# Optimization experiments

Hardware: AMD Instinct MI355X
Metric: run time of the kernel (lower is better)

## Reference

```python
import jax, jax.numpy as jnp
import numpy as np

B, IMG, TXT, DIM, H, D = 1, 1024, 256, 1536, 24, 64
SCALE = 1.0  # control cross-attn scale


def _lin(x, w, b):
    return x @ w + b


def _heads(x):  # [B,S,DIM] -> [B,H,S,D]
    return jnp.swapaxes(x.reshape(x.shape[0], x.shape[1], H, D), 1, 2)


def _merge(x):  # [B,H,S,D] -> [B,S,DIM]
    return jnp.swapaxes(x, 1, 2).reshape(x.shape[0], x.shape[2], H * D)


def _sdpa(q, k, v):
    s = jnp.einsum('bhqd,bhkd->bhqk', q, k) * (1.0 / np.sqrt(D))
    return jnp.einsum('bhqk,bhkd->bhqd', jax.nn.softmax(s, axis=-1), v)


def _rope(x, pe):  # x: [B,H,S,D], pe: [1,1,S,D//2,2,2]
    xr = x.reshape(*x.shape[:-1], -1, 1, 2)  # [B,H,S,D/2,1,2]
    out = pe[..., 0] * xr[..., 0] + pe[..., 1] * xr[..., 1]  # [B,H,S,D/2,2]
    return out.reshape(x.shape)


def _forward(hidden_states, encoder_hidden_states, hidden_states_control,
             encoder_hidden_states_control, img_to_q_control, pe,
             a_q_w, a_q_b, a_k_w, a_k_b, a_v_w, a_v_b,
             a_addq_w, a_addq_b, a_addk_w, a_addk_b, a_addv_w, a_addv_b,
             a_out_w, a_out_b, a_addout_w, a_addout_b,
             c_q_w, c_q_b, c_k_w, c_k_b, c_v_w, c_v_b,
             c_addq_w, c_addq_b, c_addk_w, c_addk_b, c_addv_w, c_addv_b,
             c_out_w, c_out_b, c_addout_w, c_addout_b):
    img_len = hidden_states.shape[1]
    # ---- main joint attention stream (no RoPE, per original) ----
    q = jnp.concatenate([_heads(_lin(hidden_states, a_q_w, a_q_b)),
                         _heads(_lin(encoder_hidden_states, a_addq_w, a_addq_b))], axis=2)
    k = jnp.concatenate([_heads(_lin(hidden_states, a_k_w, a_k_b)),
                         _heads(_lin(encoder_hidden_states, a_addk_w, a_addk_b))], axis=2)
    v = jnp.concatenate([_heads(_lin(hidden_states, a_v_w, a_v_b)),
                         _heads(_lin(encoder_hidden_states, a_addv_w, a_addv_b))], axis=2)
    hs = _merge(_sdpa(q, k, v))
    hs, ehs = hs[:, :img_len], hs[:, img_len:]
    # ---- control joint attention stream (with RoPE) ----
    qc = jnp.concatenate([_heads(_lin(hidden_states_control, c_q_w, c_q_b)),
                          _heads(_lin(encoder_hidden_states_control, c_addq_w, c_addq_b))], axis=2)
    kc = jnp.concatenate([_heads(_lin(hidden_states_control, c_k_w, c_k_b)),
                          _heads(_lin(encoder_hidden_states_control, c_addk_w, c_addk_b))], axis=2)
    vc = jnp.concatenate([_heads(_lin(hidden_states_control, c_v_w, c_v_b)),
                          _heads(_lin(encoder_hidden_states_control, c_addv_w, c_addv_b))], axis=2)
    key_cross, value_cross = kc, vc  # saved BEFORE RoPE, per original
    hsc = _merge(_sdpa(_rope(qc, pe), _rope(kc, pe), vc))
    hsc, ehsc = hsc[:, :img_len], hsc[:, img_len:]
    # ---- cross attention: img query attends to control K/V ----
    q_cross = _rope(_heads(img_to_q_control), pe[:, :, :img_len])
    k_cross = _rope(key_cross, pe[:, :, :key_cross.shape[2]])
    cross = _merge(_sdpa(q_cross, k_cross, value_cross))
    hs = hs + SCALE * cross
    # ---- output projections (to_out[1] is dropout p=0 -> identity) ----
    hs = _lin(hs, a_out_w, a_out_b)
    ehs = _lin(ehs, a_addout_w, a_addout_b)
    hsc = _lin(hsc, c_out_w, c_out_b)
    ehsc = _lin(ehsc, c_addout_w, c_addout_b)
    return hs, ehs, hsc, ehsc


def setup_inputs() -> dict:
    key = jax.random.key(0)
    ki = iter(jax.random.split(key, 80))
    d = {}
    d['hidden_states'] = jax.random.normal(next(ki), (B, IMG, DIM), jnp.float32)
    d['encoder_hidden_states'] = jax.random.normal(next(ki), (B, TXT, DIM), jnp.float32)
    d['hidden_states_control'] = jax.random.normal(next(ki), (B, IMG, DIM), jnp.float32)
    d['encoder_hidden_states_control'] = jax.random.normal(next(ki), (B, TXT, DIM), jnp.float32)
    d['img_to_q_control'] = jax.random.normal(next(ki), (B, IMG, DIM), jnp.float32)
    # realistic rotary pe: [1,1,S,D/2,2,2] rotation matrices
    S = IMG + TXT
    pos = np.arange(S, dtype=np.float32)
    freqs = 1.0 / (10000.0 ** (np.arange(0, D, 2, dtype=np.float32) / D))  # [D/2]
    ang = pos[:, None] * freqs[None, :]  # [S, D/2]
    cos, sin = np.cos(ang), np.sin(ang)
    pe = np.stack([np.stack([cos, -sin], -1), np.stack([sin, cos], -1)], -2)  # [S,D/2,2,2]
    d['pe'] = jnp.asarray(pe)[None, None]
    for p in ('a', 'c'):
        for name in ('q', 'k', 'v', 'addq', 'addk', 'addv', 'out', 'addout'):
            d[f'{p}_{name}_w'] = jax.random.normal(next(ki), (DIM, DIM), jnp.float32) * 0.02
            d[f'{p}_{name}_b'] = jax.random.normal(next(ki), (DIM,), jnp.float32) * 0.01
    return d


def reference(hidden_states, encoder_hidden_states, hidden_states_control,
              encoder_hidden_states_control, img_to_q_control, pe,
              a_q_w, a_q_b, a_k_w, a_k_b, a_v_w, a_v_b,
              a_addq_w, a_addq_b, a_addk_w, a_addk_b, a_addv_w, a_addv_b,
              a_out_w, a_out_b, a_addout_w, a_addout_b,
              c_q_w, c_q_b, c_k_w, c_k_b, c_v_w, c_v_b,
              c_addq_w, c_addq_b, c_addk_w, c_addk_b, c_addv_w, c_addv_b,
              c_out_w, c_out_b, c_addout_w, c_addout_b):
    return _forward(hidden_states, encoder_hidden_states, hidden_states_control,
                    encoder_hidden_states_control, img_to_q_control, pe,
                    a_q_w, a_q_b, a_k_w, a_k_b, a_v_w, a_v_b,
                    a_addq_w, a_addq_b, a_addk_w, a_addk_b, a_addv_w, a_addv_b,
                    a_out_w, a_out_b, a_addout_w, a_addout_b,
                    c_q_w, c_q_b, c_k_w, c_k_b, c_v_w, c_v_b,
                    c_addq_w, c_addq_b, c_addk_w, c_addk_b, c_addv_w, c_addv_b,
                    c_out_w, c_out_b, c_addout_w, c_addout_b)
```

## Files before the change

kernel.cpp:

```cpp
#include <hip/hip_runtime.h>

#define DIM 1536
#define IMG 1024
#define TXT 256
#define SEQ 1280
#define NH 24
#define HD 64
#define SD ((size_t)SEQ * DIM)
#define IDSZ ((size_t)IMG * DIM)
#define WSZ ((size_t)DIM * DIM)

typedef __attribute__((ext_vector_type(8))) short short8;
typedef __attribute__((ext_vector_type(4))) float f32x4;

__device__ __forceinline__ float bf2f(ushort u) {
    union { unsigned int i; float f; } v; v.i = ((unsigned int)u) << 16; return v.f;
}
__device__ __forceinline__ ushort f2bf(float f) {
    union { unsigned int i; float f; } v; v.f = f;
    unsigned int u = v.i;
    u += 0x7fffu + ((u >> 16) & 1u);
    return (ushort)(u >> 16);
}

__global__ __launch_bounds__(256) void detect_dtype(const void* __restrict__ p,
                                                    int* __restrict__ flag)
{
    __shared__ int cnt;
    if (threadIdx.x == 0) cnt = 0;
    __syncthreads();
    const ushort* u = (const ushort*)p;
    int local = 0;
    for (int i = threadIdx.x; i < 2048; i += 256) {
        ushort v = u[2 * i];
        int e = (v >> 7) & 0xFF;
        if (e >= 0xC0) local++;
    }
    atomicAdd(&cnt, local);
    __syncthreads();
    if (threadIdx.x == 0) flag[0] = (cnt > 16) ? 1 : 0;
}

struct CvtP {
    const void* src[20];
    ushort* dst[20];
    int n8[20];
};

__global__ __launch_bounds__(256) void convert_bf16(CvtP p, const int* __restrict__ dflag)
{
    const int a = blockIdx.y;
    const int i = blockIdx.x * 256 + threadIdx.x;
    if (i >= p.n8[a]) return;
    const size_t off = (size_t)i * 8;
    uint4 o;
    if (dflag[0]) {
        const float* s = (const float*)p.src[a] + off;
        const float4 f0 = *(const float4*)s;
        const float4 f1 = *(const float4*)(s + 4);
        ushort t[8];
        t[0] = f2bf(f0.x); t[1] = f2bf(f0.y); t[2] = f2bf(f0.z); t[3] = f2bf(f0.w);
        t[4] = f2bf(f1.x); t[5] = f2bf(f1.y); t[6] = f2bf(f1.z); t[7] = f2bf(f1.w);
        o = *(uint4*)t;
    } else {
        o = *(const uint4*)((const ushort*)p.src[a] + off);
    }
    *(uint4*)(p.dst[a] + off) = o;
}

#define LSTR 40

struct QKV3P {
    const ushort* Xb;
    const ushort* Wb;
    const void* B[12];
    float* Y[6];
    ushort* Yh[6];
    ushort* Yl[6];
};

__global__ __launch_bounds__(256) void gemm_qkv_v4(QKV3P p, const int* __restrict__ dflag)
{
    __shared__ __align__(16) ushort As[2][128 * LSTR];
    __shared__ __align__(16) ushort Bs[2][64 * 64];
    const int dt = dflag[0];
    const int bx = blockIdx.x;
    const int wsel = bx / 12;
    const int n0 = (bx - wsel * 12) * 128;
    const int ys = blockIdx.y;
    const int str = (ys >= 10) ? 1 : 0;
    const int m0g = (ys - str * 10) * 128;
    const bool istxt = (m0g >= IMG);
    const int widx = str * 6 + wsel + (istxt ? 3 : 0);
    const ushort* X  = p.Xb + (size_t)str * SD;
    const ushort* Wp = p.Wb + (size_t)widx * WSZ;
    const void* Bp = p.B[widx];
    const int yidx = str * 3 + wsel;
    float*  Y  = p.Y[yidx];
    ushort* yh = p.Yh[yidx];
    ushort* yl = p.Yl[yidx];

    const int t = threadIdx.x;
    const int wave = t >> 6, lane = t & 63;
    const int quad = lane >> 4, l16 = lane & 15;
    const int wm = (wave >> 1) * 64, wn = (wave & 1) * 64;

    const int arow = t >> 1, apair = t & 1;
    const int bn8 = (t & 15) << 3, bkk = (t >> 4) << 1;
    const int aps = apair ^ ((arow >> 3) & 1);
    const int adst = arow * LSTR + aps * 16;
    const int bkg = bkk >> 3, bo = bkk & 7;

    f32x4 acc[4][4];
#pragma unroll
    for (int i = 0; i < 4; ++i)
#pragma unroll
        for (int j = 0; j < 4; ++j) acc[i][j] = (f32x4)(0.0f);

    uint4 rau[2];
    uint4 rbu[2];

    auto loadA = [&](int k0) {
        const ushort* xp = X + (size_t)(m0g + arow) * DIM + k0 + apair * 16;
        rau[0] = *(const uint4*)xp;
        rau[1] = *(const uint4*)(xp + 8);
    };
    auto loadB = [&](int k0) {
        const ushort* wp0 = Wp + (size_t)(k0 + bkk) * DIM + n0 + bn8;
        rbu[0] = *(const uint4*)wp0;
        rbu[1] = *(const uint4*)(wp0 + DIM);
    };
    auto storeA = [&](int buf) {
        *(uint4*)&As[buf][adst]     = rau[0];
        *(uint4*)&As[buf][adst + 8] = rau[1];
    };
    auto storeB = [&](int buf) {
        ushort t0[8], t1[8];
        *(uint4*)t0 = rbu[0];
        *(uint4*)t1 = rbu[1];
#pragma unroll
        for (int j = 0; j < 8; ++j) {
            const int rr = bn8 + j;
            const int R = rr & 63, half = rr >> 6;
            const int gx = (((half << 2) + bkg) ^ (R & 7) ^ (R >> 3)) & 7;
            *(unsigned int*)&Bs[buf][R * 64 + gx * 8 + bo] =
                (unsigned int)t0[j] | ((unsigned int)t1[j] << 16);
        }
    };

    loadA(0); loadB(0);
    storeA(0); storeB(0);
    __syncthreads();

    for (int k = 0; k < DIM / 32; ++k) {
        const int cur = k & 1;
        const bool hn = (k + 1) < DIM / 32;
        if (hn) { loadA((k + 1) * 32); loadB((k + 1) * 32); }

        short8 b[4];
#pragma unroll
        for (int j = 0; j < 4; ++j) {
            const int rrn = wn + j * 16 + l16;
            const int R = rrn & 63, half = rrn >> 6;
            const int gx = (((half << 2) + quad) ^ (R & 7) ^ (R >> 3)) & 7;
            b[j] = *(const short8*)&Bs[cur][R * 64 + gx * 8];
        }
#pragma unroll
        for (int i = 0; i < 4; ++i) {
            const int rr = wm + i * 16 + l16;
            const int ps = (quad >> 1) ^ ((rr >> 3) & 1);
            const int col = ps * 16 + (quad & 1) * 8;
            short8 a = *(const short8*)&As[cur][rr * LSTR + col];
#pragma unroll
            for (int j = 0; j < 4; ++j)
                acc[i][j] = __builtin_amdgcn_mfma_f32_16x16x32_bf16(a, b[j], acc[i][j], 0, 0, 0);
        }
        if (hn) { storeA(cur ^ 1); storeB(cur ^ 1); }
        __syncthreads();
    }

#pragma unroll
    for (int j = 0; j < 4; ++j) {
        const int col = n0 + wn + j * 16 + l16;
        const float bv = dt ? ((const float*)Bp)[col] : bf2f(((const ushort*)Bp)[col]);
#pragma unroll
        for (int i = 0; i < 4; ++i)
#pragma unroll
            for (int r = 0; r < 4; ++r) {
                const int row = m0g + wm + i * 16 + quad * 4 + r;
                const size_t o = (size_t)row * DIM + col;
                const float val = acc[i][j][r] + bv;
                if (Y) Y[o] = val;
                if (yh) {
                    const ushort hv = f2bf(val);
                    yh[o] = hv;
                    yl[o] = f2bf(val - bf2f(hv));
                }
            }
    }
}

struct OutP {
    const ushort* Xh; const ushort* Xl;
    const ushort* Wb;
    const void* B[4];
    void* out;
};

__global__ __launch_bounds__(256) void gemm_out_v4(OutP p, const int* __restrict__ dflag)
{
    __shared__ __align__(16) ushort Ah[2][64 * LSTR];
    __shared__ __align__(16) ushort Al[2][64 * LSTR];
    __shared__ __align__(16) ushort Bs[2][64 * 64];
    const int dt = dflag[0];
    const int n0 = blockIdx.x * 128;
    const int mt = blockIdx.y;
    const int seg = (mt < 16) ? 0 : (mt < 20) ? 1 : (mt < 36) ? 2 : 3;
    const ushort* Wp = p.Wb + (size_t)seg * WSZ;
    const void* Bp = p.B[seg];
    const int m0 = mt * 64;

    const int t = threadIdx.x;
    const int wave = t >> 6, lane = t & 63;
    const int quad = lane >> 4, l16 = lane & 15;
    const int wm = (wave >> 1) * 32, wn = (wave & 1) * 64;

    const int arow = t >> 2, ag = t & 3;
    const int apg = ag >> 1, asub = ag & 1;
    const int aps = apg ^ ((arow >> 3) & 1);
    const int adst = arow * LSTR + aps * 16 + asub * 8;
    const int bn8 = (t & 15) << 3, bkk = (t >> 4) << 1;
    const int bkg = bkk >> 3, bo = bkk & 7;

    f32x4 acc[2][4];
#pragma unroll
    for (int i = 0; i < 2; ++i)
#pragma unroll
        for (int j = 0; j < 4; ++j) acc[i][j] = (f32x4)(0.0f);

    uint4 rah, ral;
    uint4 rbu[2];

    auto loadA = [&](int k0) {
        const size_t off = (size_t)(m0 + arow) * DIM + k0 + ag * 8;
        rah = *(const uint4*)(p.Xh + off);
        ral = *(const uint4*)(p.Xl + off);
    };
    auto loadB = [&](int k0) {
        const ushort* wp0 = Wp + (size_t)(k0 + bkk) * DIM + n0 + bn8;
        rbu[0] = *(const uint4*)wp0;
        rbu[1] = *(const uint4*)(wp0 + DIM);
    };
    auto storeA = [&](int buf) {
        *(uint4*)&Ah[buf][adst] = rah;
        *(uint4*)&Al[buf][adst] = ral;
    };
    auto storeB = [&](int buf) {
        ushort t0[8], t1[8];
        *(uint4*)t0 = rbu[0];
        *(uint4*)t1 = rbu[1];
#pragma unroll
        for (int j = 0; j < 8; ++j) {
            const int rr = bn8 + j;
            const int R = rr & 63, half = rr >> 6;
            const int gx = (((half << 2) + bkg) ^ (R & 7) ^ (R >> 3)) & 7;
            *(unsigned int*)&Bs[buf][R * 64 + gx * 8 + bo] =
                (unsigned int)t0[j] | ((unsigned int)t1[j] << 16);
        }
    };

    loadA(0); loadB(0);
    storeA(0); storeB(0);
    __syncthreads();

    for (int k = 0; k < DIM / 32; ++k) {
        const int cur = k & 1;
        const bool hn = (k + 1) < DIM / 32;
        if (hn) { loadA((k + 1) * 32); loadB((k + 1) * 32); }

        short8 b[4];
#pragma unroll
        for (int j = 0; j < 4; ++j) {
            const int rrn = wn + j * 16 + l16;
            const int R = rrn & 63, half = rrn >> 6;
            const int gx = (((half << 2) + quad) ^ (R & 7) ^ (R >> 3)) & 7;
            b[j] = *(const short8*)&Bs[cur][R * 64 + gx * 8];
        }
#pragma unroll
        for (int i = 0; i < 2; ++i) {
            const int rr = wm + i * 16 + l16;
            const int ps = (quad >> 1) ^ ((rr >> 3) & 1);
            const int col = ps * 16 + (quad & 1) * 8;
            short8 ah = *(const short8*)&Ah[cur][rr * LSTR + col];
            short8 al = *(const short8*)&Al[cur][rr * LSTR + col];
#pragma unroll
            for (int j = 0; j < 4; ++j) {
                acc[i][j] = __builtin_amdgcn_mfma_f32_16x16x32_bf16(ah, b[j], acc[i][j], 0, 0, 0);
                acc[i][j] = __builtin_amdgcn_mfma_f32_16x16x32_bf16(al, b[j], acc[i][j], 0, 0, 0);
            }
        }
        if (hn) { storeA(cur ^ 1); storeB(cur ^ 1); }
        __syncthreads();
    }

#pragma unroll
    for (int j = 0; j < 4; ++j) {
        const int col = n0 + wn + j * 16 + l16;
        const float bv = dt ? ((const float*)Bp)[col] : bf2f(((const ushort*)Bp)[col]);
#pragma unroll
        for (int i = 0; i < 2; ++i)
#pragma unroll
            for (int r = 0; r < 4; ++r) {
                const int grow = m0 + wm + i * 16 + quad * 4 + r;
                const size_t o = (size_t)grow * DIM + col;
                const float val = acc[i][j][r] + bv;
                if (dt) ((float*)p.out)[o] = val;
                else    ((ushort*)p.out)[o] = f2bf(val);
            }
    }
}

__device__ __forceinline__ void pe_load(const void* pe, int dt, size_t off,
                                        float& c00, float& c01, float& c10, float& c11)
{
    if (dt) {
        float4 pv = *(const float4*)((const float*)pe + off);
        c00 = pv.x; c01 = pv.y; c10 = pv.z; c11 = pv.w;
    } else {
        const ushort* pp = (const ushort*)pe + off;
        c00 = bf2f(pp[0]); c01 = bf2f(pp[1]); c10 = bf2f(pp[2]); c11 = bf2f(pp[3]);
    }
}

struct PrepP {
    const float* v1; const float* vC;
    ushort *vthA, *vtlA, *vthC, *vtlC;
    float* q1;
    const float* k1; ushort *khC, *kloC;
    const void* i2q; float* qx;
    const void* pe;
};

#define VT_BLKS 960
#define RN0 (SEQ * 768)
#define RN1 (SEQ * 768)
#define RN2 (IMG * 768)

__global__ __launch_bounds__(256) void prep_fused(PrepP p, const int* __restrict__ dflag)
{
    __shared__ unsigned int tile[64 * 65];
    const int dt = dflag[0];
    const int bx = blockIdx.x;
    const int t = threadIdx.x;

    if (bx < VT_BLKS) {
        const int z = bx / 480, rem = bx - z * 480;
        const int s0 = (rem % 20) * 64, h = rem / 20;
        const float* V = z ? p.vC : p.v1;
        ushort* Vth = z ? p.vthC : p.vthA;
        ushort* Vtl = z ? p.vtlC : p.vtlA;
#pragma unroll
        for (int it = 0; it < 16; ++it) {
            const int sl = (t >> 6) + (it << 2);
            const int d = t & 63;
            const float v = V[(size_t)(s0 + sl) * DIM + h * HD + d];
            const ushort hv = f2bf(v);
            const ushort lv = f2bf(v - bf2f(hv));
            tile[d * 65 + sl] = (unsigned int)hv | ((unsigned int)lv << 16);
        }
        __syncthreads();
        const int d = t >> 2, cc = (t & 3) << 4;
        ushort th[16], tl[16];
#pragma unroll
        for (int j = 0; j < 16; ++j) {
            const unsigned int w = tile[d * 65 + cc + j];
            th[j] = (ushort)w;
            tl[j] = (ushort)(w >> 16);
        }
        const size_t off = (size_t)(h * HD + d) * SEQ + s0 + cc;
        *(uint4*)(Vth + off)     = *(uint4*)&th[0];
        *(uint4*)(Vth + off + 8) = *(uint4*)&th[8];
        *(uint4*)(Vtl + off)     = *(uint4*)&tl[0];
        *(uint4*)(Vtl + off + 8) = *(uint4*)&tl[8];
        return;
    }

    int idx = (bx - VT_BLKS) * 256 + t;
    if (idx < RN0) {
        int s = idx / 768, pp = idx - s * 768;
        int col = pp << 1, i = pp & 31;
        float* bp = p.q1 + (size_t)s * DIM + col;
        float x0 = bp[0], x1 = bp[1];
        float c00, c01, c10, c11;
        pe_load(p.pe, dt, (size_t)s * 128 + i * 4, c00, c01, c10, c11);
        bp[0] = c00 * x0 + c01 * x1;
        bp[1] = c10 * x0 + c11 * x1;
        return;
    }
    idx -= RN0;
    if (idx < RN1) {
        int s = idx / 768, pp = idx - s * 768;
        int col = pp << 1, i = pp & 31;
        float2 xv = *(const float2*)(p.k1 + (size_t)s * DIM + col);
        float c00, c01, c10, c11;
        pe_load(p.pe, dt, (size_t)s * 128 + i * 4, c00, c01, c10, c11);
        float y0 = c00 * xv.x + c01 * xv.y;
        float y1 = c10 * xv.x + c11 * xv.y;
        ushort h0 = f2bf(y0), h1 = f2bf(y1);
        ushort l0 = f2bf(y0 - bf2f(h0)), l1 = f2bf(y1 - bf2f(h1));
        *(unsigned int*)(p.khC  + (size_t)s * DIM + col) = (unsigned int)h0 | ((unsigned int)h1 << 16);
        *(unsigned int*)(p.kloC + (size_t)s * DIM + col) = (unsigned int)l0 | ((unsigned int)l1 << 16);
        return;
    }
    idx -= RN1;
    if (idx < RN2) {
        int s = idx / 768, pp = idx - s * 768;
        int col = pp << 1, i = pp & 31;
        float x0, x1;
        if (dt) {
            float2 xv = *(const float2*)((const float*)p.i2q + (size_t)s * DIM + col);
            x0 = xv.x; x1 = xv.y;
        } else {
            const ushort* sp = (const ushort*)p.i2q + (size_t)s * DIM + col;
            x0 = bf2f(sp[0]); x1 = bf2f(sp[1]);
        }
        float c00, c01, c10, c11;
        pe_load(p.pe, dt, (size_t)s * 128 + i * 4, c00, c01, c10, c11);
        float* dp = p.qx + (size_t)s * DIM + col;
        dp[0] = c00 * x0 + c01 * x1;
        dp[1] = c10 * x0 + c11 * x1;
    }
}

__device__ __forceinline__ int swz(int row, int col) {
    return row * 64 + ((((col >> 3) ^ row) & 7) << 3) + (col & 7);
}
__device__ __forceinline__ short8 ldfrag(const ushort* plane, int row, int col) {
    return *(const short8*)&plane[swz(row, col)];
}

struct AttnAllP {
    const float* Qf[3];
    const ushort* Kh[3]; const ushort* Kl[3];
    const ushort* Vth[3]; const ushort* Vtl[3];
    float* Op0[3]; float* Op1[3];
    float2* Ml[3];
    int mlq[3];
};

__global__ __launch_bounds__(256) void attn_all(AttnAllP p)
{
    __shared__ ushort Qh_[4096], Ql_[4096];
    __shared__ ushort Kh_[4096], Kl_[4096];
    __shared__ ushort Vh_[4096], Vl_[4096];

    const int bx = blockIdx.x;
    const int seg = (bx < 20) ? 0 : (bx < 40) ? 1 : 2;
    const int q0 = (bx - ((seg == 0) ? 0 : (seg == 1) ? 20 : 40)) * 64;
    const int h = blockIdx.y;
    const int z = blockIdx.z;
    const int t = threadIdx.x;
    const int wave = t >> 6, lane = t & 63;
    const int quad = lane >> 4, l16 = lane & 15;
    const int wq0 = wave * 16;

    const float* Qf = p.Qf[seg];
    const ushort* Kh = p.Kh[seg]; const ushort* Kl = p.Kl[seg];
    const ushort* Vth = p.Vth[seg]; const ushort* Vtl = p.Vtl[seg];

    const int srow = t >> 2, c0 = (t & 3) << 4;
    const int g0 = c0 >> 3;
    const int p0 = ((g0 ^ (srow & 7)) & 7) << 3;
    const int p1 = (((g0 + 1) ^ (srow & 7)) & 7) << 3;

    {
        const float* src = Qf + (size_t)(q0 + srow) * DIM + h * HD + c0;
        float x[16];
        *(float4*)&x[0]  = *(const float4*)(src);
        *(float4*)&x[4]  = *(const float4*)(src + 4);
        *(float4*)&x[8]  = *(const float4*)(src + 8);
        *(float4*)&x[12] = *(const float4*)(src + 12);
        ushort hi[16], lo[16];
#pragma unroll
        for (int i = 0; i < 16; ++i) {
            hi[i] = f2bf(x[i]);
            lo[i] = f2bf(x[i] - bf2f(hi[i]));
        }
        *(uint4*)&Qh_[srow * 64 + p0] = *(uint4*)&hi[0];
        *(uint4*)&Qh_[srow * 64 + p1] = *(uint4*)&hi[8];
        *(uint4*)&Ql_[srow * 64 + p0] = *(uint4*)&lo[0];
        *(uint4*)&Ql_[srow * 64 + p1] = *(uint4*)&lo[8];
    }
    short8 qfh[2], qfl[2];
#pragma unroll
    for (int c = 0; c < 2; ++c) {
        qfh[c] = ldfrag(Qh_, wq0 + l16, c * 32 + quad * 8);
        qfl[c] = ldfrag(Ql_, wq0 + l16, c * 32 + quad * 8);
    }

    float m_[4], l_[4];
#pragma unroll
    for (int r = 0; r < 4; ++r) { m_[r] = -3e38f; l_[r] = 0.0f; }
    f32x4 Oacc[4];
#pragma unroll
    for (int j = 0; j < 4; ++j) Oacc[j] = (f32x4)(0.0f);

    const int kvbeg = z * (SEQ / 2);
    for (int kt = 0; kt < SEQ / 2; kt += 64) {
        const int kv0 = kvbeg + kt;
        __syncthreads();
        {
            const size_t off = (size_t)(kv0 + srow) * DIM + h * HD + c0;
            *(uint4*)&Kh_[srow * 64 + p0] = *(const uint4*)(Kh + off);
            *(uint4*)&Kh_[srow * 64 + p1] = *(const uint4*)(Kh + off + 8);
            *(uint4*)&Kl_[srow * 64 + p0] = *(const uint4*)(Kl + off);
            *(uint4*)&Kl_[srow * 64 + p1] = *(const uint4*)(Kl + off + 8);
        }
        {
            const size_t off = (size_t)(h * HD + srow) * SEQ + kv0 + c0;
            *(uint4*)&Vh_[srow * 64 + p0] = *(const uint4*)(Vth + off);
            *(uint4*)&Vh_[srow * 64 + p1] = *(const uint4*)(Vth + off + 8);
            *(uint4*)&Vl_[srow * 64 + p0] = *(const uint4*)(Vtl + off);
            *(uint4*)&Vl_[srow * 64 + p1] = *(const uint4*)(Vtl + off + 8);
        }
        __syncthreads();

        f32x4 S[4];
#pragma unroll
        for (int j = 0; j < 4; ++j) S[j] = (f32x4)(0.0f);
        __builtin_amdgcn_s_setprio(1);
#pragma unroll
        for (int c = 0; c < 2; ++c) {
#pragma unroll
            for (int j = 0; j < 4; ++j) {
                short8 bh = ldfrag(Kh_, j * 16 + l16, c * 32 + quad * 8);
                short8 bl = ldfrag(Kl_, j * 16 + l16, c * 32 + quad * 8);
                S[j] = __builtin_amdgcn_mfma_f32_16x16x32_bf16(qfh[c], bh, S[j], 0, 0, 0);
                S[j] = __builtin_amdgcn_mfma_f32_16x16x32_bf16(qfl[c], bh, S[j], 0, 0, 0);
                S[j] = __builtin_amdgcn_mfma_f32_16x16x32_bf16(qfh[c], bl, S[j], 0, 0, 0);
            }
        }
        __builtin_amdgcn_s_setprio(0);
#pragma unroll
        for (int j = 0; j < 4; ++j)
#pragma unroll
            for (int r = 0; r < 4; ++r) S[j][r] *= 0.125f;

        float alpha[4];
#pragma unroll
        for (int r = 0; r < 4; ++r) {
            float mx = fmaxf(fmaxf(S[0][r], S[1][r]), fmaxf(S[2][r], S[3][r]));
            mx = fmaxf(mx, __shfl_xor(mx, 1));
            mx = fmaxf(mx, __shfl_xor(mx, 2));
            mx = fmaxf(mx, __shfl_xor(mx, 4));
            mx = fmaxf(mx, __shfl_xor(mx, 8));
            float mn = fmaxf(m_[r], mx);
            alpha[r] = __expf(m_[r] - mn);
            m_[r] = mn;
            float rs = 0.0f;
#pragma unroll
            for (int j = 0; j < 4; ++j) {
                float pv = __expf(S[j][r] - mn);
                S[j][r] = pv;
                rs += pv;
            }
            rs += __shfl_xor(rs, 1);
            rs += __shfl_xor(rs, 2);
            rs += __shfl_xor(rs, 4);
            rs += __shfl_xor(rs, 8);
            l_[r] = l_[r] * alpha[r] + rs;
        }
#pragma unroll
        for (int j = 0; j < 4; ++j)
#pragma unroll
            for (int r = 0; r < 4; ++r) Oacc[j][r] *= alpha[r];

        {
            const int prow = wq0 + quad * 4;
#pragma unroll
            for (int j = 0; j < 4; ++j)
#pragma unroll
                for (int r = 0; r < 4; ++r) {
                    float pv = S[j][r];
                    ushort ph = f2bf(pv);
                    ushort pl = f2bf(pv - bf2f(ph));
                    int idx = swz(prow + r, j * 16 + l16);
                    Qh_[idx] = ph;
                    Ql_[idx] = pl;
                }
        }

        __builtin_amdgcn_s_setprio(1);
#pragma unroll
        for (int c = 0; c < 2; ++c) {
            short8 pah = ldfrag(Qh_, wq0 + l16, c * 32 + quad * 8);
            short8 pal = ldfrag(Ql_, wq0 + l16, c * 32 + quad * 8);
#pragma unroll
            for (int jn = 0; jn < 4; ++jn) {
                short8 vbh = ldfrag(Vh_, jn * 16 + l16, c * 32 + quad * 8);
                short8 vbl = ldfrag(Vl_, jn * 16 + l16, c * 32 + quad * 8);
                Oacc[jn] = __builtin_amdgcn_mfma_f32_16x16x32_bf16(pah, vbh, Oacc[jn], 0, 0, 0);
                Oacc[jn] = __builtin_amdgcn_mfma_f32_16x16x32_bf16(pal, vbh, Oacc[jn], 0, 0, 0);
                Oacc[jn] = __builtin_amdgcn_mfma_f32_16x16x32_bf16(pah, vbl, Oacc[jn], 0, 0, 0);
            }
        }
        __builtin_amdgcn_s_setprio(0);
    }

    float* Opz = z ? p.Op1[seg] : p.Op0[seg];
    const int mlq = p.mlq[seg];
    float2* Ml = p.Ml[seg];
#pragma unroll
    for (int r = 0; r < 4; ++r) {
        const int rowq = q0 + wq0 + quad * 4 + r;
        if (l16 == 0)
            Ml[((size_t)z * NH + h) * mlq + rowq] = make_float2(m_[r], l_[r]);
#pragma unroll
        for (int jn = 0; jn < 4; ++jn)
            Opz[(size_t)rowq * DIM + h * HD + jn * 16 + l16] = Oacc[jn][r];
    }
}

struct MergeP {
    const float *pA0, *pA1, *pC0, *pC1, *pX0, *pX1;
    const float2 *MlA, *MlC, *MlX;
    ushort *Xh, *Xl;
};

__device__ __forceinline__ float4 comb2(const float* O0, const float* O1,
                                        const float2* Ml, int mlq, int row, int c4)
{
    const int h = c4 >> 6;
    const float2 a = Ml[(size_t)h * mlq + row];
    const float2 b = Ml[(size_t)(NH + h) * mlq + row];
    const float ms = fmaxf(a.x, b.x);
    const float s0 = __expf(a.x - ms), s1 = __expf(b.x - ms);
    const float inv = 1.0f / (s0 * a.y + s1 * b.y);
    const float4 o0 = *(const float4*)&O0[(size_t)row * DIM + c4];
    const float4 o1 = *(const float4*)&O1[(size_t)row * DIM + c4];
    float4 r;
    r.x = (s0 * o0.x + s1 * o1.x) * inv;
    r.y = (s0 * o0.y + s1 * o1.y) * inv;
    r.z = (s0 * o0.z + s1 * o1.z) * inv;
    r.w = (s0 * o0.w + s1 * o1.w) * inv;
    return r;
}

__global__ __launch_bounds__(256) void merge_all(MergeP p)
{
    const int idx = blockIdx.x * 256 + threadIdx.x;
    if (idx >= 2560 * 384) return;
    const int row = idx / 384;
    const int c4 = (idx - row * 384) << 2;
    float4 r;
    if (row < SEQ) {
        r = comb2(p.pA0, p.pA1, p.MlA, SEQ, row, c4);
        if (row < IMG) {
            const float4 x = comb2(p.pX0, p.pX1, p.MlX, IMG, row, c4);
            r.x += x.x; r.y += x.y; r.z += x.z; r.w += x.w;
        }
    } else {
        r = comb2(p.pC0, p.pC1, p.MlC, SEQ, row - SEQ, c4);
    }
    float v[4] = {r.x, r.y, r.z, r.w};
    ushort hi[4], lo[4];
#pragma unroll
    for (int j = 0; j < 4; ++j) {
        hi[j] = f2bf(v[j]);
        lo[j] = f2bf(v[j] - bf2f(hi[j]));
    }
    const size_t o = (size_t)row * DIM + c4;
    *(uint2*)(p.Xh + o) = *(uint2*)hi;
    *(uint2*)(p.Xl + o) = *(uint2*)lo;
}

extern "C" void kernel_launch(void* const* d_in, const int* in_sizes, int n_in,
                              void* d_out, int out_size, void* d_ws, size_t ws_size,
                              hipStream_t stream) {
    (void)in_sizes; (void)n_in; (void)out_size; (void)ws_size;
    const void* hs   = d_in[0];
    const void* ehs  = d_in[1];
    const void* hsc  = d_in[2];
    const void* ehsc = d_in[3];
    const void* i2q  = d_in[4];
    const void* pe   = d_in[5];
#define W_(i) ((const void*)d_in[i])

    char* base = (char*)d_ws;
    int* flag = (int*)base;
    char* ptr = base + 256;
    auto alloc = [&](size_t bytes) { char* r = ptr; ptr += bytes; return r; };
    float* q1  = (float*)alloc(SD * 4);
    float* k1  = (float*)alloc(SD * 4);
    float* v1  = (float*)alloc(SD * 4);
    float* vC  = (float*)alloc(SD * 4);
    float* qA  = (float*)alloc(SD * 4);
    float* qx  = (float*)alloc(IDSZ * 4);
    ushort* khA  = (ushort*)alloc(SD * 2);
    ushort* kloA = (ushort*)alloc(SD * 2);
    ushort* vthA = (ushort*)alloc(SD * 2);
    ushort* vtlA = (ushort*)alloc(SD * 2);
    ushort* khC  = (ushort*)alloc(SD * 2);
    ushort* kloC = (ushort*)alloc(SD * 2);
    ushort* vthC = (ushort*)alloc(SD * 2);
    ushort* vtlC = (ushort*)alloc(SD * 2);
    float* pX0 = (float*)alloc(IDSZ * 4);
    float* pX1 = (float*)alloc(IDSZ * 4);
    float2* MlA = (float2*)alloc((size_t)2 * NH * SEQ * 8);
    float2* MlC = (float2*)alloc((size_t)2 * NH * SEQ * 8);
    float2* MlX = (float2*)alloc((size_t)2 * NH * IMG * 8);
    ushort* Wbf = (ushort*)alloc(16 * WSZ * 2);
    ushort* Xbf = (ushort*)alloc(2 * SD * 2);
    float* pC1 = (float*)Xbf;
    ushort* Xh = (ushort*)qA;
    ushort* Xl = (ushort*)q1;

    dim3 blk(256);
    detect_dtype<<<1, blk, 0, stream>>>(hs, flag);

    {
        CvtP cp;
        const int wsrc[16] = {6, 8, 10, 12, 14, 16, 22, 24, 26, 28, 30, 32,
                              18, 20, 34, 36};
        for (int j = 0; j < 16; ++j) {
            cp.src[j] = W_(wsrc[j]);
            cp.dst[j] = Wbf + (size_t)j * WSZ;
            cp.n8[j] = (int)(WSZ / 8);
        }
        cp.src[16] = hs;   cp.dst[16] = Xbf;             cp.n8[16] = (int)(IDSZ / 8);
        cp.src[17] = ehs;  cp.dst[17] = Xbf + IDSZ;      cp.n8[17] = (int)((size_t)TXT * DIM / 8);
        cp.src[18] = hsc;  cp.dst[18] = Xbf + SD;        cp.n8[18] = (int)(IDSZ / 8);
        cp.src[19] = ehsc; cp.dst[19] = Xbf + SD + IDSZ; cp.n8[19] = (int)((size_t)TXT * DIM / 8);
        convert_bf16<<<dim3((int)(WSZ / 8 + 255) / 256, 20), blk, 0, stream>>>(cp, flag);
    }

    QKV3P qp;
    qp.Xb = Xbf;
    qp.Wb = Wbf;
    {
        const int bsrc[12] = {7, 9, 11, 13, 15, 17, 23, 25, 27, 29, 31, 33};
        for (int j = 0; j < 12; ++j) qp.B[j] = W_(bsrc[j]);
    }
    for (int j = 0; j < 6; ++j) { qp.Y[j] = nullptr; qp.Yh[j] = nullptr; qp.Yl[j] = nullptr; }
    qp.Y[0] = qA;
    qp.Yh[1] = khA; qp.Yl[1] = kloA;
    qp.Y[2] = v1;
    qp.Y[3] = q1;
    qp.Y[4] = k1;
    qp.Y[5] = vC;
    gemm_qkv_v4<<<dim3(36, 20), blk, 0, stream>>>(qp, flag);

    {
        PrepP pp;
        pp.v1 = v1; pp.vC = vC;
        pp.vthA = vthA; pp.vtlA = vtlA; pp.vthC = vthC; pp.vtlC = vtlC;
        pp.q1 = q1;
        pp.k1 = k1; pp.khC = khC; pp.kloC = kloC;
        pp.i2q = i2q; pp.qx = qx;
        pp.pe = pe;
        const int ropeBlocks = (RN0 + RN1 + RN2 + 255) / 256;
        prep_fused<<<VT_BLKS + ropeBlocks, blk, 0, stream>>>(pp, flag);
    }

    {
        AttnAllP ap;
        ap.Qf[0] = qA; ap.Qf[1] = q1; ap.Qf[2] = qx;
        ap.Kh[0] = khA; ap.Kl[0] = kloA;
        ap.Kh[1] = khC; ap.Kl[1] = kloC;
        ap.Kh[2] = khC; ap.Kl[2] = kloC;
        ap.Vth[0] = vthA; ap.Vtl[0] = vtlA;
        ap.Vth[1] = vthC; ap.Vtl[1] = vtlC;
        ap.Vth[2] = vthC; ap.Vtl[2] = vtlC;
        ap.Op0[0] = v1;  ap.Op1[0] = k1;
        ap.Op0[1] = vC;  ap.Op1[1] = pC1;
        ap.Op0[2] = pX0; ap.Op1[2] = pX1;
        ap.Ml[0] = MlA; ap.Ml[1] = MlC; ap.Ml[2] = MlX;
        ap.mlq[0] = SEQ; ap.mlq[1] = SEQ; ap.mlq[2] = IMG;
        attn_all<<<dim3(56, NH, 2), blk, 0, stream>>>(ap);
    }

    {
        MergeP mp;
        mp.pA0 = v1; mp.pA1 = k1;
        mp.pC0 = vC; mp.pC1 = pC1;
        mp.pX0 = pX0; mp.pX1 = pX1;
        mp.MlA = MlA; mp.MlC = MlC; mp.MlX = MlX;
        mp.Xh = Xh; mp.Xl = Xl;
        merge_all<<<(2560 * 384 + 255) / 256, blk, 0, stream>>>(mp);
    }

    {
        OutP op;
        op.Xh = Xh; op.Xl = Xl;
        op.Wb = Wbf + (size_t)12 * WSZ;
        op.B[0] = W_(19); op.B[1] = W_(21); op.B[2] = W_(35); op.B[3] = W_(37);
        op.out = d_out;
        gemm_out_v4<<<dim3(12, 40), blk, 0, stream>>>(op, flag);
    }
#undef W_
}
```

Baseline: 555.0 us.

## Prefetch next K/V tile into registers, fold softmax scale into Q, pack bf16 conversions

The attention kernel now issues global loads for the next K/V tile into registers before computing on the current tile, then writes them to shared memory after the PV matmul. This hides global memory latency behind MFMA work. It also folds the 1/sqrt(D) scale into Q at load time, precomputes the swizzled LDS offsets, and uses the v_cvt_pk_bf16_f32 instruction for the hi/lo split of P. The costs are extra registers for the prefetch buffers (with launch bounds set to 3 blocks per CU) and a change in rounding from scaling before the split, plus the packed convert's rounding mode.

```diff
diff --git a/kernel.cpp b/kernel.cpp
--- a/kernel.cpp
+++ b/kernel.cpp
@@ -21,6 +21,11 @@
     unsigned int u = v.i;
     u += 0x7fffu + ((u >> 16) & 1u);
     return (ushort)(u >> 16);
+}
+__device__ __forceinline__ unsigned int cvtpk(float a, float b) {
+    unsigned int r;
+    asm("v_cvt_pk_bf16_f32 %0, %1, %2" : "=v"(r) : "v"(a), "v"(b));
+    return r;
 }
 
 __global__ __launch_bounds__(256) void detect_dtype(const void* __restrict__ p,
@@ -435,9 +440,6 @@
 __device__ __forceinline__ int swz(int row, int col) {
     return row * 64 + ((((col >> 3) ^ row) & 7) << 3) + (col & 7);
 }
-__device__ __forceinline__ short8 ldfrag(const ushort* plane, int row, int col) {
-    return *(const short8*)&plane[swz(row, col)];
-}
 
 struct AttnAllP {
     const float* Qf[3];
@@ -448,7 +450,9 @@
     int mlq[3];
 };
 
-__global__ __launch_bounds__(256) void attn_all(AttnAllP p)
+#define NKT 10
+
+__global__ __launch_bounds__(256, 3) void attn_all(AttnAllP p)
 {
     __shared__ ushort Qh_[4096], Ql_[4096];
     __shared__ ushort Kh_[4096], Kl_[4096];
@@ -473,6 +477,23 @@
     const int p0 = ((g0 ^ (srow & 7)) & 7) << 3;
     const int p1 = (((g0 + 1) ^ (srow & 7)) & 7) << 3;
 
+    int offF[2];
+    int offB2[4][2];
+#pragma unroll
+    for (int c = 0; c < 2; ++c) {
+        offF[c] = swz(wq0 + l16, c * 32 + quad * 8);
+#pragma unroll
+        for (int j = 0; j < 4; ++j)
+            offB2[j][c] = swz(j * 16 + l16, c * 32 + quad * 8);
+    }
+    const int prow = wq0 + quad * 4;
+    int pidx[4][4];
+#pragma unroll
+    for (int j = 0; j < 4; ++j)
+#pragma unroll
+        for (int r = 0; r < 4; ++r)
+            pidx[j][r] = swz(prow + r, j * 16 + l16);
+
     {
         const float* src = Qf + (size_t)(q0 + srow) * DIM + h * HD + c0;
         float x[16];
@@ -483,8 +504,9 @@
         ushort hi[16], lo[16];
 #pragma unroll
         for (int i = 0; i < 16; ++i) {
-            hi[i] = f2bf(x[i]);
-            lo[i] = f2bf(x[i] - bf2f(hi[i]));
+            const float xs = x[i] * 0.125f;
+            hi[i] = f2bf(xs);
+            lo[i] = f2bf(xs - bf2f(hi[i]));
         }
         *(uint4*)&Qh_[srow * 64 + p0] = *(uint4*)&hi[0];
         *(uint4*)&Qh_[srow * 64 + p1] = *(uint4*)&hi[8];
@@ -494,8 +516,8 @@
     short8 qfh[2], qfl[2];
 #pragma unroll
     for (int c = 0; c < 2; ++c) {
-        qfh[c] = ldfrag(Qh_, wq0 + l16, c * 32 + quad * 8);
-        qfl[c] = ldfrag(Ql_, wq0 + l16, c * 32 + quad * 8);
+        qfh[c] = *(const short8*)&Qh_[offF[c]];
+        qfl[c] = *(const short8*)&Ql_[offF[c]];
     }
 
     float m_[4], l_[4];
@@ -506,24 +528,38 @@
     for (int j = 0; j < 4; ++j) Oacc[j] = (f32x4)(0.0f);
 
     const int kvbeg = z * (SEQ / 2);
-    for (int kt = 0; kt < SEQ / 2; kt += 64) {
-        const int kv0 = kvbeg + kt;
-        __syncthreads();
-        {
-            const size_t off = (size_t)(kv0 + srow) * DIM + h * HD + c0;
-            *(uint4*)&Kh_[srow * 64 + p0] = *(const uint4*)(Kh + off);
-            *(uint4*)&Kh_[srow * 64 + p1] = *(const uint4*)(Kh + off + 8);
-            *(uint4*)&Kl_[srow * 64 + p0] = *(const uint4*)(Kl + off);
-            *(uint4*)&Kl_[srow * 64 + p1] = *(const uint4*)(Kl + off + 8);
-        }
-        {
-            const size_t off = (size_t)(h * HD + srow) * SEQ + kv0 + c0;
-            *(uint4*)&Vh_[srow * 64 + p0] = *(const uint4*)(Vth + off);
-            *(uint4*)&Vh_[srow * 64 + p1] = *(const uint4*)(Vth + off + 8);
-            *(uint4*)&Vl_[srow * 64 + p0] = *(const uint4*)(Vtl + off);
-            *(uint4*)&Vl_[srow * 64 + p1] = *(const uint4*)(Vtl + off + 8);
-        }
-        __syncthreads();
+
+    uint4 rk[4], rv[4];
+    auto loadKV = [&](int kv0) {
+        const size_t ko = (size_t)(kv0 + srow) * DIM + h * HD + c0;
+        rk[0] = *(const uint4*)(Kh + ko);
+        rk[1] = *(const uint4*)(Kh + ko + 8);
+        rk[2] = *(const uint4*)(Kl + ko);
+        rk[3] = *(const uint4*)(Kl + ko + 8);
+        const size_t vo = (size_t)(h * HD + srow) * SEQ + kv0 + c0;
+        rv[0] = *(const uint4*)(Vth + vo);
+        rv[1] = *(const uint4*)(Vth + vo + 8);
+        rv[2] = *(const uint4*)(Vtl + vo);
+        rv[3] = *(const uint4*)(Vtl + vo + 8);
+    };
+    auto writeKV = [&]() {
+        *(uint4*)&Kh_[srow * 64 + p0] = rk[0];
+        *(uint4*)&Kh_[srow * 64 + p1] = rk[1];
+        *(uint4*)&Kl_[srow * 64 + p0] = rk[2];
+        *(uint4*)&Kl_[srow * 64 + p1] = rk[3];
+        *(uint4*)&Vh_[srow * 64 + p0] = rv[0];
+        *(uint4*)&Vh_[srow * 64 + p1] = rv[1];
+        *(uint4*)&Vl_[srow * 64 + p0] = rv[2];
+        *(uint4*)&Vl_[srow * 64 + p1] = rv[3];
+    };
+
+    loadKV(kvbeg);
+    writeKV();
+    __syncthreads();
+
+    for (int kt = 0; kt < NKT; ++kt) {
+        const bool hn = (kt + 1) < NKT;
+        if (hn) loadKV(kvbeg + (kt + 1) * 64);
 
         f32x4 S[4];
 #pragma unroll
@@ -533,18 +569,14 @@
         for (int c = 0; c < 2; ++c) {
 #pragma unroll
             for (int j = 0; j < 4; ++j) {
-                short8 bh = ldfrag(Kh_, j * 16 + l16, c * 32 + quad * 8);
-                short8 bl = ldfrag(Kl_, j * 16 + l16, c * 32 + quad * 8);
+                short8 bh = *(const short8*)&Kh_[offB2[j][c]];
+                short8 bl = *(const short8*)&Kl_[offB2[j][c]];
                 S[j] = __builtin_amdgcn_mfma_f32_16x16x32_bf16(qfh[c], bh, S[j], 0, 0, 0);
                 S[j] = __builtin_amdgcn_mfma_f32_16x16x32_bf16(qfl[c], bh, S[j], 0, 0, 0);
                 S[j] = __builtin_amdgcn_mfma_f32_16x16x32_bf16(qfh[c], bl, S[j], 0, 0, 0);
             }
         }
         __builtin_amdgcn_s_setprio(0);
-#pragma unroll
-        for (int j = 0; j < 4; ++j)
-#pragma unroll
-            for (int r = 0; r < 4; ++r) S[j][r] *= 0.125f;
 
         float alpha[4];
 #pragma unroll
@@ -575,36 +607,46 @@
 #pragma unroll
             for (int r = 0; r < 4; ++r) Oacc[j][r] *= alpha[r];
 
-        {
-            const int prow = wq0 + quad * 4;
-#pragma unroll
-            for (int j = 0; j < 4; ++j)
-#pragma unroll
-                for (int r = 0; r < 4; ++r) {
-                    float pv = S[j][r];
-                    ushort ph = f2bf(pv);
-                    ushort pl = f2bf(pv - bf2f(ph));
-                    int idx = swz(prow + r, j * 16 + l16);
-                    Qh_[idx] = ph;
-                    Ql_[idx] = pl;
-                }
+#pragma unroll
+        for (int j = 0; j < 4; ++j) {
+            const unsigned int h01 = cvtpk(S[j][0], S[j][1]);
+            const unsigned int h23 = cvtpk(S[j][2], S[j][3]);
+            union { unsigned int u; float f; } b0, b1, b2, b3;
+            b0.u = h01 << 16; b1.u = h01 & 0xffff0000u;
+            b2.u = h23 << 16; b3.u = h23 & 0xffff0000u;
+            const unsigned int l01 = cvtpk(S[j][0] - b0.f, S[j][1] - b1.f);
+            const unsigned int l23 = cvtpk(S[j][2] - b2.f, S[j][3] - b3.f);
+            Qh_[pidx[j][0]] = (ushort)h01;
+            Qh_[pidx[j][1]] = (ushort)(h01 >> 16);
+            Qh_[pidx[j][2]] = (ushort)h23;
+            Qh_[pidx[j][3]] = (ushort)(h23 >> 16);
+            Ql_[pidx[j][0]] = (ushort)l01;
+            Ql_[pidx[j][1]] = (ushort)(l01 >> 16);
+            Ql_[pidx[j][2]] = (ushort)l23;
+            Ql_[pidx[j][3]] = (ushort)(l23 >> 16);
         }
 
         __builtin_amdgcn_s_setprio(1);
 #pragma unroll
         for (int c = 0; c < 2; ++c) {
-            short8 pah = ldfrag(Qh_, wq0 + l16, c * 32 + quad * 8);
-            short8 pal = ldfrag(Ql_, wq0 + l16, c * 32 + quad * 8);
+            short8 pah = *(const short8*)&Qh_[offF[c]];
+            short8 pal = *(const short8*)&Ql_[offF[c]];
 #pragma unroll
             for (int jn = 0; jn < 4; ++jn) {
-                short8 vbh = ldfrag(Vh_, jn * 16 + l16, c * 32 + quad * 8);
-                short8 vbl = ldfrag(Vl_, jn * 16 + l16, c * 32 + quad * 8);
+                short8 vbh = *(const short8*)&Vh_[offB2[jn][c]];
+                short8 vbl = *(const short8*)&Vl_[offB2[jn][c]];
                 Oacc[jn] = __builtin_amdgcn_mfma_f32_16x16x32_bf16(pah, vbh, Oacc[jn], 0, 0, 0);
                 Oacc[jn] = __builtin_amdgcn_mfma_f32_16x16x32_bf16(pal, vbh, Oacc[jn], 0, 0, 0);
                 Oacc[jn] = __builtin_amdgcn_mfma_f32_16x16x32_bf16(pah, vbl, Oacc[jn], 0, 0, 0);
             }
         }
         __builtin_amdgcn_s_setprio(0);
+
+        if (hn) {
+            __syncthreads();
+            writeKV();
+            __syncthreads();
+        }
     }
 
     float* Opz = z ? p.Op1[seg] : p.Op0[seg];
```

New measurement: 680.2 us. 1.23x slower.
